# Optimization experiments

Measured on AMD Instinct MI355X. Metric: run time of the kernel, lower is better.

The kernel has to match this reference:

```python
import jax, jax.numpy as jnp
import numpy as np

B, T, D, H = 2, 2048, 1024, 16
DH = D // H


def setup_inputs() -> dict:
    key = jax.random.key(0)
    ks = jax.random.split(key, 5)
    scale = 1.0 / np.sqrt(D)
    return {
        "x": jax.random.normal(ks[0], (B, T, D), dtype=jnp.float32),
        "Wq": jax.random.normal(ks[1], (D, D), dtype=jnp.float32) * scale,
        "Wk": jax.random.normal(ks[2], (D, D), dtype=jnp.float32) * scale,
        "Wv": jax.random.normal(ks[3], (D, D), dtype=jnp.float32) * scale,
        "Wo": jax.random.normal(ks[4], (D, D), dtype=jnp.float32) * scale,
    }


def _split(y):
    # (B,T,D) -> (B,H,T,DH)
    b, t, _ = y.shape
    return y.reshape(b, t, H, DH).transpose(0, 2, 1, 3)


def reference(x, Wq, Wk, Wv, Wo):
    q = _split(x @ Wq)
    k = _split(x @ Wk)
    v = _split(x @ Wv)
    scores = jnp.einsum("bhqd,bhkd->bhqk", q, k) / jnp.sqrt(jnp.float32(DH))
    t = x.shape[1]
    # additive causal mask: -1e9 above the diagonal (matches band_part logic)
    causal = jnp.tril(jnp.ones((t, t), dtype=jnp.float32))
    scores = scores + (1.0 - causal) * -1e9
    attn = jax.nn.softmax(scores, axis=-1)
    out = jnp.einsum("bhqk,bhkd->bhqd", attn, v)  # (B,H,T,DH)
    out = out.transpose(0, 2, 1, 3).reshape(x.shape[0], t, D)
    return out @ Wo
```

## Files before the change

### kernel.cpp

```cpp
#include <hip/hip_runtime.h>

#define BB 2
#define TT 2048
#define DD 1024
#define HH 16
#define DHD 64
#define MM (BB*TT)

typedef __attribute__((ext_vector_type(8))) short short8;
typedef __attribute__((ext_vector_type(4))) float float4v;
typedef unsigned short u16;

__device__ inline float bf2f(u16 u) {
    union { unsigned int i; float f; } v;
    v.i = ((unsigned int)u) << 16;
    return v.f;
}
__device__ inline u16 f2bf(float f) {
    union { float f; unsigned int i; } v;
    v.f = f;
    unsigned int x = v.i;
    unsigned int r = (x + 0x7fffu + ((x >> 16) & 1u)) >> 16;
    return (u16)r;
}

__global__ __launch_bounds__(256) void cast_x_k(const float* __restrict__ x,
                                                u16* __restrict__ xb) {
    int i = blockIdx.x * 256 + threadIdx.x;
    float4v v = ((const float4v*)x)[i];
    ushort4 o;
    o.x = f2bf(v[0]); o.y = f2bf(v[1]); o.z = f2bf(v[2]); o.w = f2bf(v[3]);
    ((ushort4*)xb)[i] = o;
}

__global__ __launch_bounds__(256) void transw_k(const float* __restrict__ Wq,
                                                const float* __restrict__ Wk,
                                                const float* __restrict__ Wv,
                                                const float* __restrict__ Wo,
                                                u16* __restrict__ WT) {
    __shared__ u16 t[32][33];
    int wsel = blockIdx.z;
    const float* W = (wsel == 0) ? Wq : (wsel == 1) ? Wk : (wsel == 2) ? Wv : Wo;
    u16* o = WT + (size_t)wsel * DD * DD;
    int k0 = blockIdx.y * 32, n0 = blockIdx.x * 32;
    int tx = threadIdx.x, ty = threadIdx.y;
#pragma unroll
    for (int i = 0; i < 4; i++) {
        int k = ty + i * 8;
        t[k][tx] = f2bf(W[(size_t)(k0 + k) * DD + n0 + tx]);
    }
    __syncthreads();
#pragma unroll
    for (int i = 0; i < 4; i++) {
        int n = ty + i * 8;
        o[(size_t)(n0 + n) * DD + k0 + tx] = t[tx][n];
    }
}

template <int MODE, int TM, int TN>
__global__ __launch_bounds__(256) void gemm_k(const u16* __restrict__ A,
                                              const u16* __restrict__ WT0,
                                              void* __restrict__ outp) {
    const int K = DD, BK = 64;
    const int MT = TM / 32, NT = TN / 32;
    const int NS = (TM + TN) * (BK / 8) / 256;

    int z = blockIdx.z;
    const u16* WT = WT0 + (size_t)z * DD * DD;
    int n0 = blockIdx.x * TN, m0 = blockIdx.y * TM;

    __shared__ u16 S[(TM + TN) * BK];

    int tid = threadIdx.x;
    int lane = tid & 63, w = tid >> 6;
    int wm = (w >> 1) * (TM / 2), wn = (w & 1) * (TN / 2);
    int quad = lane >> 4, l16 = lane & 15;

    const u16* gp[NS];
    u16* lp[NS];
#pragma unroll
    for (int j = 0; j < NS; j++) {
        int cid = tid + j * 256;
        int r = cid >> 3, c = cid & 7;
        lp[j] = S + r * BK + (c ^ (r & 7)) * 8;
        gp[j] = (r < TM ? A + (size_t)(m0 + r) * K
                        : WT + (size_t)(n0 + r - TM) * K) + c * 8;
    }
    int swz = l16 & 7;

    float4v acc[MT][NT];
#pragma unroll
    for (int i = 0; i < MT; i++)
#pragma unroll
        for (int j = 0; j < NT; j++) acc[i][j] = (float4v)(0.0f);

    short8 pr[NS];
#pragma unroll
    for (int j = 0; j < NS; j++) pr[j] = *(const short8*)gp[j];

    const int NK = K / BK;
#pragma unroll 1
    for (int ki = 0; ki < NK; ki++) {
        __syncthreads();
#pragma unroll
        for (int j = 0; j < NS; j++) *(short8*)lp[j] = pr[j];
        __syncthreads();

        if (ki + 1 < NK) {
            int k0 = (ki + 1) * BK;
#pragma unroll
            for (int j = 0; j < NS; j++) pr[j] = *(const short8*)(gp[j] + k0);
        }

#pragma unroll
        for (int ks = 0; ks < 2; ks++) {
            int cq = ((ks * 4 + quad) ^ swz) * 8;
            short8 a[MT], b[NT];
#pragma unroll
            for (int mt = 0; mt < MT; mt++)
                a[mt] = *(const short8*)&S[(wm + mt * 16 + l16) * BK + cq];
#pragma unroll
            for (int nt = 0; nt < NT; nt++)
                b[nt] = *(const short8*)&S[(TM + wn + nt * 16 + l16) * BK + cq];
#pragma unroll
            for (int mt = 0; mt < MT; mt++)
#pragma unroll
                for (int nt = 0; nt < NT; nt++)
                    acc[mt][nt] = __builtin_amdgcn_mfma_f32_16x16x32_bf16(
                        a[mt], b[nt], acc[mt][nt], 0, 0, 0);
        }
    }

#pragma unroll
    for (int mt = 0; mt < MT; mt++) {
#pragma unroll
        for (int nt = 0; nt < NT; nt++) {
#pragma unroll
            for (int r = 0; r < 4; r++) {
                int m = m0 + wm + mt * 16 + quad * 4 + r;
                int n = n0 + wn + nt * 16 + l16;
                float v = acc[mt][nt][r];
                if constexpr (MODE == 0) {
                    int bb = m >> 11, t = m & 2047;
                    int h = n >> 6, dh = n & 63;
                    size_t idx;
                    if (z == 2)
                        idx = (((size_t)2 * BB * HH + bb * HH + h) * DHD + dh) * TT + t;
                    else
                        idx = (((size_t)z * BB * HH + bb * HH + h) * TT + t) * DHD + dh;
                    ((u16*)outp)[idx] = f2bf(v);
                } else {
                    ((float*)outp)[(size_t)m * DD + n] = v;
                }
            }
        }
    }
}

__global__ __launch_bounds__(512) void attn_k(const u16* __restrict__ QKV,
                                              u16* __restrict__ AO) {
    const u16* Q  = QKV;
    const u16* Kp = QKV + (size_t)MM * DD;
    const u16* Vp = QKV + (size_t)2 * MM * DD;
    int bh = blockIdx.y;
    int tswz = (blockIdx.x + blockIdx.y) & 15;
    int p = (blockIdx.y & 16) ? (15 - tswz) : tswz;
    int qA = p, qB = 31 - p;
    size_t hoff = (size_t)bh * TT * DHD;

    __shared__ u16 Ks[2][64 * 64];
    __shared__ u16 VTs[2][64 * 64];
    __shared__ u16 Ps[8][16 * 64];

    int tid = threadIdx.x;
    int lane = tid & 63, wv = tid >> 6;
    int g = wv >> 2, w4 = wv & 3;
    int quad = lane >> 4, l16 = lane & 15;

    int sr = tid >> 3, sc = tid & 7;
    int sl = sr * 64 + ((sc ^ (sr & 7)) * 8);
    const u16* gK = Kp + hoff + (size_t)sr * DHD + sc * 8;
    const u16* gV = Vp + hoff + (size_t)sr * TT + sc * 8;

    u16* Qstage = &Ps[0][0];

    const float qscale = 0.125f * 1.4426950408889634f;
#pragma unroll
    for (int t = 0; t < 2; t++) {
        int q0 = (t ? qB : qA) * 64;
        short8 v = *(const short8*)(Q + hoff + (size_t)(q0 + sr) * DHD + sc * 8);
        short8 sv;
#pragma unroll
        for (int e = 0; e < 8; e++) sv[e] = (short)f2bf(bf2f((u16)v[e]) * qscale);
        *(short8*)&Qstage[t * 4096 + sl] = sv;
    }

    short8 prK = *(const short8*)gK;
    short8 prV = *(const short8*)gV;

    __syncthreads();
    int cxs = l16 & 7;
    int fr = w4 * 16 + l16;
    short8 aq0 = *(const short8*)&Qstage[g * 4096 + fr * 64 + ((quad ^ cxs) * 8)];
    short8 aq1 = *(const short8*)&Qstage[g * 4096 + fr * 64 + (((4 + quad) ^ cxs) * 8)];

    int myqt = g ? qB : qA;
    int ntile = myqt + 1;
    int NR = qB + 1;

    float4v o[4];
#pragma unroll
    for (int i = 0; i < 4; i++) o[i] = (float4v)(0.0f);
    float lr = 0.0f;

#pragma unroll 1
    for (int jt = 0; jt < NR; jt++) {
        int db = jt & 1;
        *(short8*)&Ks[db][sl]  = prK;
        *(short8*)&VTs[db][sl] = prV;
        __syncthreads();

        if (jt + 1 < NR) {
            size_t nj = (size_t)(jt + 1) * 64;
            prK = *(const short8*)(gK + nj * DHD);
            prV = *(const short8*)(gV + nj);
        }

        if (jt < ntile) {
            float4v s[4];
#pragma unroll
            for (int ct = 0; ct < 4; ct++) {
                int kr = (ct * 16 + l16) * 64;
                short8 ak0 = *(const short8*)&Ks[db][kr + ((quad ^ cxs) * 8)];
                short8 ak1 = *(const short8*)&Ks[db][kr + (((4 + quad) ^ cxs) * 8)];
                float4v sv = (float4v)(0.0f);
                sv = __builtin_amdgcn_mfma_f32_16x16x32_bf16(ak0, aq0, sv, 0, 0, 0);
                sv = __builtin_amdgcn_mfma_f32_16x16x32_bf16(ak1, aq1, sv, 0, 0, 0);
                s[ct] = sv;
            }

            if (jt == myqt) {
                int ql = w4 * 16 + l16;
#pragma unroll
                for (int ct = 0; ct < 4; ct++)
#pragma unroll
                    for (int r = 0; r < 4; r++) {
                        int kvl = ct * 16 + quad * 4 + r;
                        if (kvl > ql) s[ct][r] = -30000.0f;
                    }
            }

#pragma unroll
            for (int ct = 0; ct < 4; ct++) {
                float p0 = exp2f(s[ct][0]);
                float p1 = exp2f(s[ct][1]);
                float p2 = exp2f(s[ct][2]);
                float p3 = exp2f(s[ct][3]);
                lr += (p0 + p1) + (p2 + p3);
                union { float f; unsigned u; } c0, c1, c2, c3;
                c0.f = p0; c1.f = p1; c2.f = p2; c3.f = p3;
                uint2 pw;
                pw.x = __builtin_amdgcn_perm(c1.u, c0.u, 0x07060302u);
                pw.y = __builtin_amdgcn_perm(c3.u, c2.u, 0x07060302u);
                int chnk = (ct * 2 + (quad >> 1)) ^ cxs;
                *(uint2*)&Ps[wv][l16 * 64 + chnk * 8 + (quad & 1) * 4] = pw;
            }

            short8 ap0 = *(const short8*)&Ps[wv][l16 * 64 + ((quad ^ cxs) * 8)];
            short8 ap1 = *(const short8*)&Ps[wv][l16 * 64 + (((4 + quad) ^ cxs) * 8)];
#pragma unroll
            for (int ct = 0; ct < 4; ct++) {
                int vr = (ct * 16 + l16) * 64;
                short8 bv0 = *(const short8*)&VTs[db][vr + ((quad ^ cxs) * 8)];
                short8 bv1 = *(const short8*)&VTs[db][vr + (((4 + quad) ^ cxs) * 8)];
                o[ct] = __builtin_amdgcn_mfma_f32_16x16x32_bf16(ap0, bv0, o[ct], 0, 0, 0);
                o[ct] = __builtin_amdgcn_mfma_f32_16x16x32_bf16(ap1, bv1, o[ct], 0, 0, 0);
            }
        }
    }

    float rs = lr;
    rs += __shfl_xor(rs, 16);
    rs += __shfl_xor(rs, 32);
    int gbase = lane & 48;
    float rinv[4];
#pragma unroll
    for (int r = 0; r < 4; r++)
        rinv[r] = 1.0f / __shfl(rs, gbase + quad * 4 + r);

    int b = bh >> 4, h = bh & 15;
    int q0 = myqt * 64;
#pragma unroll
    for (int ct = 0; ct < 4; ct++) {
#pragma unroll
        for (int r = 0; r < 4; r++) {
            int q = q0 + w4 * 16 + quad * 4 + r;
            int d = h * 64 + ct * 16 + l16;
            AO[(size_t)(b * TT + q) * DD + d] = f2bf(o[ct][r] * rinv[r]);
        }
    }
}

extern "C" void kernel_launch(void* const* d_in, const int* in_sizes, int n_in,
                              void* d_out, int out_size, void* d_ws, size_t ws_size,
                              hipStream_t stream) {
    const float* x  = (const float*)d_in[0];
    const float* Wq = (const float*)d_in[1];
    const float* Wk = (const float*)d_in[2];
    const float* Wv = (const float*)d_in[3];
    const float* Wo = (const float*)d_in[4];

    u16* xb  = (u16*)d_ws;
    u16* WT  = xb + (size_t)MM * DD;
    u16* QKV = WT + (size_t)4 * DD * DD;
    u16* AO  = QKV + (size_t)3 * MM * DD;
    float* out = (float*)d_out;

    cast_x_k<<<dim3(MM * DD / 1024), 256, 0, stream>>>(x, xb);
    transw_k<<<dim3(32, 32, 4), dim3(32, 8), 0, stream>>>(Wq, Wk, Wv, Wo, WT);
    gemm_k<0, 128, 128><<<dim3(DD / 128, MM / 128, 3), 256, 0, stream>>>(xb, WT, QKV);
    attn_k<<<dim3(16, 32), 512, 0, stream>>>(QKV, AO);
    gemm_k<1, 64, 128><<<dim3(DD / 128, MM / 64, 1), 256, 0, stream>>>(AO, WT + (size_t)3 * DD * DD, out);
}
```

Measured before the change: 176.4 us.

## Give each attention wave 32 query rows to reuse K/V fragments

Attention blocks shrink from 8 waves to 4, and each wave now handles two 16-row query subtiles instead of one. Each K and V^T fragment read from LDS then feeds two MFMAs, which halves LDS reads per FLOP and halves the number of waves sharing the block. Each thread now stages two rows of K/V per tile. In exchange it uses more registers per wave for the doubled accumulators and scores, and has fewer waves per block to hide latency.

```diff
diff --git a/kernel.cpp b/kernel.cpp
--- a/kernel.cpp
+++ b/kernel.cpp
@@ -157,7 +157,7 @@
     }
 }
 
-__global__ __launch_bounds__(512) void attn_k(const u16* __restrict__ QKV,
+__global__ __launch_bounds__(256) void attn_k(const u16* __restrict__ QKV,
                                               u16* __restrict__ AO) {
     const u16* Q  = QKV;
     const u16* Kp = QKV + (size_t)MM * DD;
@@ -170,15 +170,17 @@
 
     __shared__ u16 Ks[2][64 * 64];
     __shared__ u16 VTs[2][64 * 64];
-    __shared__ u16 Ps[8][16 * 64];
+    __shared__ u16 Ps[4][32 * 64];
 
     int tid = threadIdx.x;
     int lane = tid & 63, wv = tid >> 6;
-    int g = wv >> 2, w4 = wv & 3;
+    int g = wv >> 1, h16 = wv & 1;
     int quad = lane >> 4, l16 = lane & 15;
+    int cxs = l16 & 7;
 
     int sr = tid >> 3, sc = tid & 7;
-    int sl = sr * 64 + ((sc ^ (sr & 7)) * 8);
+    int swc = (sc ^ (sr & 7)) * 8;
+    int sl0 = sr * 64 + swc, sl1 = (sr + 32) * 64 + swc;
     const u16* gK = Kp + hoff + (size_t)sr * DHD + sc * 8;
     const u16* gV = Vp + hoff + (size_t)sr * TT + sc * 8;
 
@@ -188,115 +190,149 @@
 #pragma unroll
     for (int t = 0; t < 2; t++) {
         int q0 = (t ? qB : qA) * 64;
-        short8 v = *(const short8*)(Q + hoff + (size_t)(q0 + sr) * DHD + sc * 8);
-        short8 sv;
-#pragma unroll
-        for (int e = 0; e < 8; e++) sv[e] = (short)f2bf(bf2f((u16)v[e]) * qscale);
-        *(short8*)&Qstage[t * 4096 + sl] = sv;
-    }
-
-    short8 prK = *(const short8*)gK;
-    short8 prV = *(const short8*)gV;
+#pragma unroll
+        for (int jj = 0; jj < 2; jj++) {
+            int r = sr + jj * 32;
+            short8 v = *(const short8*)(Q + hoff + (size_t)(q0 + r) * DHD + sc * 8);
+            short8 sv;
+#pragma unroll
+            for (int e = 0; e < 8; e++) sv[e] = (short)f2bf(bf2f((u16)v[e]) * qscale);
+            *(short8*)&Qstage[t * 4096 + r * 64 + swc] = sv;
+        }
+    }
+
+    short8 prK0 = *(const short8*)gK;
+    short8 prK1 = *(const short8*)(gK + (size_t)32 * DHD);
+    short8 prV0 = *(const short8*)gV;
+    short8 prV1 = *(const short8*)(gV + (size_t)32 * TT);
 
     __syncthreads();
-    int cxs = l16 & 7;
-    int fr = w4 * 16 + l16;
-    short8 aq0 = *(const short8*)&Qstage[g * 4096 + fr * 64 + ((quad ^ cxs) * 8)];
-    short8 aq1 = *(const short8*)&Qstage[g * 4096 + fr * 64 + (((4 + quad) ^ cxs) * 8)];
+    short8 aq[2][2];
+#pragma unroll
+    for (int qh = 0; qh < 2; qh++)
+#pragma unroll
+        for (int ks = 0; ks < 2; ks++)
+            aq[qh][ks] = *(const short8*)&Qstage[g * 4096 +
+                (h16 * 32 + qh * 16 + l16) * 64 + (((ks * 4 + quad) ^ cxs) * 8)];
 
     int myqt = g ? qB : qA;
     int ntile = myqt + 1;
     int NR = qB + 1;
 
-    float4v o[4];
-#pragma unroll
-    for (int i = 0; i < 4; i++) o[i] = (float4v)(0.0f);
-    float lr = 0.0f;
+    float4v o[2][4];
+#pragma unroll
+    for (int i = 0; i < 2; i++)
+#pragma unroll
+        for (int j = 0; j < 4; j++) o[i][j] = (float4v)(0.0f);
+    float lr[2] = {0.0f, 0.0f};
 
 #pragma unroll 1
     for (int jt = 0; jt < NR; jt++) {
         int db = jt & 1;
-        *(short8*)&Ks[db][sl]  = prK;
-        *(short8*)&VTs[db][sl] = prV;
+        *(short8*)&Ks[db][sl0]  = prK0;
+        *(short8*)&Ks[db][sl1]  = prK1;
+        *(short8*)&VTs[db][sl0] = prV0;
+        *(short8*)&VTs[db][sl1] = prV1;
         __syncthreads();
 
         if (jt + 1 < NR) {
             size_t nj = (size_t)(jt + 1) * 64;
-            prK = *(const short8*)(gK + nj * DHD);
-            prV = *(const short8*)(gV + nj);
+            prK0 = *(const short8*)(gK + nj * DHD);
+            prK1 = *(const short8*)(gK + (nj + 32) * DHD);
+            prV0 = *(const short8*)(gV + nj);
+            prV1 = *(const short8*)(gV + (size_t)32 * TT + nj);
         }
 
         if (jt < ntile) {
-            float4v s[4];
+            float4v s[2][4];
 #pragma unroll
             for (int ct = 0; ct < 4; ct++) {
                 int kr = (ct * 16 + l16) * 64;
                 short8 ak0 = *(const short8*)&Ks[db][kr + ((quad ^ cxs) * 8)];
                 short8 ak1 = *(const short8*)&Ks[db][kr + (((4 + quad) ^ cxs) * 8)];
-                float4v sv = (float4v)(0.0f);
-                sv = __builtin_amdgcn_mfma_f32_16x16x32_bf16(ak0, aq0, sv, 0, 0, 0);
-                sv = __builtin_amdgcn_mfma_f32_16x16x32_bf16(ak1, aq1, sv, 0, 0, 0);
-                s[ct] = sv;
+#pragma unroll
+                for (int qh = 0; qh < 2; qh++) {
+                    float4v sv = (float4v)(0.0f);
+                    sv = __builtin_amdgcn_mfma_f32_16x16x32_bf16(ak0, aq[qh][0], sv, 0, 0, 0);
+                    sv = __builtin_amdgcn_mfma_f32_16x16x32_bf16(ak1, aq[qh][1], sv, 0, 0, 0);
+                    s[qh][ct] = sv;
+                }
             }
 
             if (jt == myqt) {
-                int ql = w4 * 16 + l16;
-#pragma unroll
-                for (int ct = 0; ct < 4; ct++)
-#pragma unroll
-                    for (int r = 0; r < 4; r++) {
-                        int kvl = ct * 16 + quad * 4 + r;
-                        if (kvl > ql) s[ct][r] = -30000.0f;
-                    }
-            }
-
-#pragma unroll
-            for (int ct = 0; ct < 4; ct++) {
-                float p0 = exp2f(s[ct][0]);
-                float p1 = exp2f(s[ct][1]);
-                float p2 = exp2f(s[ct][2]);
-                float p3 = exp2f(s[ct][3]);
-                lr += (p0 + p1) + (p2 + p3);
-                union { float f; unsigned u; } c0, c1, c2, c3;
-                c0.f = p0; c1.f = p1; c2.f = p2; c3.f = p3;
-                uint2 pw;
-                pw.x = __builtin_amdgcn_perm(c1.u, c0.u, 0x07060302u);
-                pw.y = __builtin_amdgcn_perm(c3.u, c2.u, 0x07060302u);
-                int chnk = (ct * 2 + (quad >> 1)) ^ cxs;
-                *(uint2*)&Ps[wv][l16 * 64 + chnk * 8 + (quad & 1) * 4] = pw;
-            }
-
-            short8 ap0 = *(const short8*)&Ps[wv][l16 * 64 + ((quad ^ cxs) * 8)];
-            short8 ap1 = *(const short8*)&Ps[wv][l16 * 64 + (((4 + quad) ^ cxs) * 8)];
-#pragma unroll
-            for (int ct = 0; ct < 4; ct++) {
-                int vr = (ct * 16 + l16) * 64;
+#pragma unroll
+                for (int qh = 0; qh < 2; qh++) {
+                    int ql = h16 * 32 + qh * 16 + l16;
+#pragma unroll
+                    for (int ct = 0; ct < 4; ct++)
+#pragma unroll
+                        for (int r = 0; r < 4; r++) {
+                            int kvl = ct * 16 + quad * 4 + r;
+                            if (kvl > ql) s[qh][ct][r] = -30000.0f;
+                        }
+                }
+            }
+
+#pragma unroll
+            for (int qh = 0; qh < 2; qh++) {
+#pragma unroll
+                for (int ct = 0; ct < 4; ct++) {
+                    float p0 = exp2f(s[qh][ct][0]);
+                    float p1 = exp2f(s[qh][ct][1]);
+                    float p2 = exp2f(s[qh][ct][2]);
+                    float p3 = exp2f(s[qh][ct][3]);
+                    lr[qh] += (p0 + p1) + (p2 + p3);
+                    union { float f; unsigned u; } c0, c1, c2, c3;
+                    c0.f = p0; c1.f = p1; c2.f = p2; c3.f = p3;
+                    uint2 pw;
+                    pw.x = __builtin_amdgcn_perm(c1.u, c0.u, 0x07060302u);
+                    pw.y = __builtin_amdgcn_perm(c3.u, c2.u, 0x07060302u);
+                    int chnk = (ct * 2 + (quad >> 1)) ^ cxs;
+                    *(uint2*)&Ps[wv][(qh * 16 + l16) * 64 + chnk * 8 + (quad & 1) * 4] = pw;
+                }
+            }
+
+            short8 ap[2][2];
+#pragma unroll
+            for (int qh = 0; qh < 2; qh++)
+#pragma unroll
+                for (int ks = 0; ks < 2; ks++)
+                    ap[qh][ks] = *(const short8*)&Ps[wv][(qh * 16 + l16) * 64 +
+                                                         (((ks * 4 + quad) ^ cxs) * 8)];
+#pragma unroll
+            for (int dt = 0; dt < 4; dt++) {
+                int vr = (dt * 16 + l16) * 64;
                 short8 bv0 = *(const short8*)&VTs[db][vr + ((quad ^ cxs) * 8)];
                 short8 bv1 = *(const short8*)&VTs[db][vr + (((4 + quad) ^ cxs) * 8)];
-                o[ct] = __builtin_amdgcn_mfma_f32_16x16x32_bf16(ap0, bv0, o[ct], 0, 0, 0);
-                o[ct] = __builtin_amdgcn_mfma_f32_16x16x32_bf16(ap1, bv1, o[ct], 0, 0, 0);
-            }
-        }
-    }
-
-    float rs = lr;
-    rs += __shfl_xor(rs, 16);
-    rs += __shfl_xor(rs, 32);
-    int gbase = lane & 48;
-    float rinv[4];
-#pragma unroll
-    for (int r = 0; r < 4; r++)
-        rinv[r] = 1.0f / __shfl(rs, gbase + quad * 4 + r);
+#pragma unroll
+                for (int qh = 0; qh < 2; qh++) {
+                    o[qh][dt] = __builtin_amdgcn_mfma_f32_16x16x32_bf16(ap[qh][0], bv0, o[qh][dt], 0, 0, 0);
+                    o[qh][dt] = __builtin_amdgcn_mfma_f32_16x16x32_bf16(ap[qh][1], bv1, o[qh][dt], 0, 0, 0);
+                }
+            }
+        }
+    }
 
     int b = bh >> 4, h = bh & 15;
     int q0 = myqt * 64;
-#pragma unroll
-    for (int ct = 0; ct < 4; ct++) {
-#pragma unroll
-        for (int r = 0; r < 4; r++) {
-            int q = q0 + w4 * 16 + quad * 4 + r;
-            int d = h * 64 + ct * 16 + l16;
-            AO[(size_t)(b * TT + q) * DD + d] = f2bf(o[ct][r] * rinv[r]);
+    int gbase = lane & 48;
+#pragma unroll
+    for (int qh = 0; qh < 2; qh++) {
+        float rs = lr[qh];
+        rs += __shfl_xor(rs, 16);
+        rs += __shfl_xor(rs, 32);
+        float rinv[4];
+#pragma unroll
+        for (int r = 0; r < 4; r++)
+            rinv[r] = 1.0f / __shfl(rs, gbase + quad * 4 + r);
+#pragma unroll
+        for (int dt = 0; dt < 4; dt++) {
+#pragma unroll
+            for (int r = 0; r < 4; r++) {
+                int q = q0 + h16 * 32 + qh * 16 + quad * 4 + r;
+                int d = h * 64 + dt * 16 + l16;
+                AO[(size_t)(b * TT + q) * DD + d] = f2bf(o[qh][dt][r] * rinv[r]);
+            }
         }
     }
 }
@@ -319,6 +355,6 @@
     cast_x_k<<<dim3(MM * DD / 1024), 256, 0, stream>>>(x, xb);
     transw_k<<<dim3(32, 32, 4), dim3(32, 8), 0, stream>>>(Wq, Wk, Wv, Wo, WT);
     gemm_k<0, 128, 128><<<dim3(DD / 128, MM / 128, 3), 256, 0, stream>>>(xb, WT, QKV);
-    attn_k<<<dim3(16, 32), 512, 0, stream>>>(QKV, AO);
+    attn_k<<<dim3(16, 32), 256, 0, stream>>>(QKV, AO);
     gemm_k<1, 64, 128><<<dim3(DD / 128, MM / 64, 1), 256, 0, stream>>>(AO, WT + (size_t)3 * DD * DD, out);
 }
```

Measured after the change: 190.4 us. 7.9% more time.
